# Optimization experiments

Measured on AMD Instinct MI355X. Metric: run time of the kernel, lower is better.

The kernel has to match this reference:

```python
import jax, jax.numpy as jnp
import numpy as np

B, H, E, V = 128, 1024, 1024, 40000
L, S, A = 256, 10, 10
L_S, L_A = 1.0, 1.0  # s_copy_lambda / a_copy_lambda
NEG = -1e24


def setup_inputs():
    key = jax.random.key(0)
    ks = jax.random.split(key, 32)
    n = lambda i, shape: jax.random.normal(ks[i], shape, dtype=jnp.float32)
    p = lambda i, shape: jax.random.normal(ks[i], shape, dtype=jnp.float32) * 0.02
    rnn_in = 3 * E + H  # embed + history ctx (H) + state ctx (E) + action ctx (E)
    return {
        "inp": n(0, (B, 1, E)),
        "hidden": n(1, (1, B, H)),
        "hs_vectors": n(2, (B, L, H)),
        "state_gumbel_prob": jax.random.uniform(ks[3], (B, S, V), dtype=jnp.float32),
        "state_gumbel_embed": n(4, (B, S, E)),
        "action_gumbel_prob": jax.random.uniform(ks[5], (B, A, V), dtype=jnp.float32),
        "action_gumbel_embed": n(6, (B, A, E)),
        "history_lens": jax.random.randint(ks[7], (B,), 1, L + 1),
        "history_word_indices": jax.random.randint(ks[8], (B, L), 0, V),
        # history word mlp-attention
        "Wq_hist": p(9, (H, H)), "bq_hist": jnp.zeros((H,), jnp.float32),
        "Wm_hist": p(10, (H, H)), "v_hist": p(11, (H,)),
        # init_s_attn / init_a_attn (query H, memory E)
        "Wq_s": p(12, (H, H)), "bq_s": jnp.zeros((H,), jnp.float32),
        "Wm_s": p(13, (E, H)), "v_s": p(14, (H,)),
        "Wq_a": p(15, (H, H)), "bq_a": jnp.zeros((H,), jnp.float32),
        "Wm_a": p(16, (E, H)), "v_a": p(17, (H,)),
        # sparse_copy_attn (memory E+1)
        "Wq_sc": p(18, (H, H)), "bq_sc": jnp.zeros((H,), jnp.float32),
        "Wm_sc": p(19, (E + 1, H)), "v_sc": p(20, (H,)),
        # GRU (torch layout: [3H, in], gate order r,z,n)
        "W_ih": p(21, (3 * H, rnn_in)), "W_hh": p(22, (3 * H, H)),
        "b_ih": jnp.zeros((3 * H,), jnp.float32), "b_hh": jnp.zeros((3 * H,), jnp.float32),
        # output projection
        "W_out": p(23, (H, V)), "b_out": jnp.zeros((V,), jnp.float32),
    }


def _mlp_scores(q, mem, Wq, bq, Wm, v):
    # q: [B,1,H], mem: [B,L,M] -> additive-attention logits [B,1,L]
    t = jnp.tanh((q @ Wq + bq) + (mem @ Wm))  # [B,L,H]
    return (t @ v)[:, None, :]


def reference(inp, hidden, hs_vectors, state_gumbel_prob, state_gumbel_embed,
              action_gumbel_prob, action_gumbel_embed, history_lens,
              history_word_indices, Wq_hist, bq_hist, Wm_hist, v_hist,
              Wq_s, bq_s, Wm_s, v_s, Wq_a, bq_a, Wm_a, v_a,
              Wq_sc, bq_sc, Wm_sc, v_sc, W_ih, W_hh, b_ih, b_hh, W_out, b_out):
    q0 = jnp.transpose(hidden, (1, 0, 2))  # [B,1,H]
    # --- history word attention (masked mlp attention) ---
    hist_scores = _mlp_scores(q0, hs_vectors, Wq_hist, bq_hist, Wm_hist, v_hist)
    valid = jnp.arange(L)[None, None, :] < history_lens[:, None, None]
    hist_scores = jnp.where(valid, hist_scores, NEG)
    c_his = jax.nn.softmax(hist_scores, axis=-1) @ hs_vectors  # [B,1,H]
    # --- init_consult over state / action gumbel embeddings ---
    sw = jax.nn.softmax(_mlp_scores(q0, state_gumbel_embed, Wq_s, bq_s, Wm_s, v_s), axis=-1)
    c_state = sw @ state_gumbel_embed  # [B,1,E]
    aw = jax.nn.softmax(_mlp_scores(q0, action_gumbel_embed, Wq_a, bq_a, Wm_a, v_a), axis=-1)
    c_action = aw @ action_gumbel_embed  # [B,1,E]
    x = jnp.concatenate([inp, c_his, c_state, c_action], axis=-1)[:, 0, :]  # [B,3E+H]
    # --- single-step GRU cell (torch semantics, gate order r,z,n) ---
    h0 = hidden[0]
    gi = x @ W_ih.T + b_ih
    gh = h0 @ W_hh.T + b_hh
    ir, iz, inn = jnp.split(gi, 3, axis=-1)
    hr, hz, hn = jnp.split(gh, 3, axis=-1)
    r = jax.nn.sigmoid(ir + hr)
    z = jax.nn.sigmoid(iz + hz)
    nact = jnp.tanh(inn + r * hn)
    h_new = (1.0 - z) * nact + z * h0  # [B,H]
    # --- vocab logits + copy logits, joint softmax ---
    gene_logits = h_new @ W_out + b_out  # [B,V]
    cq = h_new[:, None, :]
    hs_logits = jnp.einsum('bqh,blh->bql', cq, hs_vectors)[:, 0, :]  # dot attn, [B,L]
    s_tag = jnp.zeros((B, S, 1), jnp.float32)
    a_tag = jnp.ones((B, A, 1), jnp.float32)
    st_logits = _mlp_scores(cq, jnp.concatenate([state_gumbel_embed, s_tag], -1), Wq_sc, bq_sc, Wm_sc, v_sc)[:, 0, :]
    ac_logits = _mlp_scores(cq, jnp.concatenate([action_gumbel_embed, a_tag], -1), Wq_sc, bq_sc, Wm_sc, v_sc)[:, 0, :]
    all_logits = jnp.concatenate([gene_logits, hs_logits, st_logits, ac_logits], axis=-1)
    wp = jax.nn.softmax(all_logits, axis=-1)  # [B, V+L+S+A]
    gene_p = wp[:, :V]
    hs_w = wp[:, V:V + L]
    st_w = wp[:, V + L:V + L + S]
    ac_w = wp[:, V + L + S:]
    # --- copy-distribution mixing ---
    scp = jnp.einsum('bs,bsv->bv', st_w, state_gumbel_prob)
    acp = jnp.einsum('ba,bav->bv', ac_w, action_gumbel_prob)
    gene_p = gene_p + L_S * scp + L_A * acp
    copy_p = jnp.zeros((B, V), jnp.float32).at[jnp.arange(B)[:, None], history_word_indices].add(hs_w)
    out = jnp.log(gene_p + copy_p)[:, None, :]  # [B,1,V]
    return out, h_new[None]
```

## Files before the change

### kernel.cpp

```cpp
#include <hip/hip_runtime.h>
#include <stdint.h>

typedef __attribute__((ext_vector_type(4))) float f32x4;
typedef __attribute__((ext_vector_type(2))) unsigned int u32x2;
typedef __attribute__((ext_vector_type(4))) unsigned int u32x4;
typedef __attribute__((ext_vector_type(8))) short bf16x8;

#define BV (128*40000)

__device__ __forceinline__ unsigned rne_bf16(float f) {
    unsigned x = __float_as_uint(f);
    return ((x + 0x7FFFu + ((x >> 16) & 1u)) >> 16) & 0xFFFFu;
}
__device__ __forceinline__ unsigned pack2(float a, float b) {
    return rne_bf16(a) | (rne_bf16(b) << 16);
}
__device__ __forceinline__ float bf2f(unsigned u) {
    return __uint_as_float((u & 0xFFFFu) << 16);
}
__device__ __forceinline__ float sigm(float x) { return 1.0f / (1.0f + expf(-x)); }
__device__ __forceinline__ float ftanh(float x) {
    float e = __expf(2.0f * x);
    return 1.0f - 2.0f / (e + 1.0f);
}
// ... 7 lines not shown
struct BigArgs {
    const unsigned short *hs, *WmhT, *se, *ae, *WmsT, *WmaT, *WmscT;
    const float *qh_h, *bq_h, *v_h;
    const float *qh_s, *bq_s, *v_s;
    const float *qh_a, *bq_a, *v_a;
    float *hsc, *stsc, *acsc;
    unsigned short *mseh, *maeh;
};

__global__ __launch_bounds__(512, 1) void k_big(
    BigArgs a, int* __restrict__ ctr, const int* __restrict__ prefix,
    const int* __restrict__ ntp) {
    __shared__ unsigned short As[2][16384];
    __shared__ unsigned short Bs[2][16384];
    __shared__ int sTile;
    __shared__ int rows_tab[256];

    const int nTiles = ntp[0], Mp = ntp[1];
    const int t = threadIdx.x, lane = t & 63, wv = t >> 6;
    const int l16 = lane & 15, lq = lane >> 4;
    const int wm = wv >> 2, wn = wv & 3;
    const int srowL = t >> 3;
    const int gccA = ((t & 7) ^ (srowL & 7)) << 3;
    const int swz = l16 & 7;
    const int c0 = ((lq ^ swz) << 3);
    const int A0 = (wm << 13) + (l16 << 6);
    const int B0 = ((wn >> 1) << 13) + ((((wn & 1) << 6) + l16) << 6);

#define STQA(ktt, d, q) gload16(gAr[q] + (ktt) * 64, &As[d][((q) << 12) + (wv << 9)])
#define STQB(ktt, d, q) gload16(gB + ((size_t)(q) << 16) + (ktt) * 64, &Bs[d][((q) << 12) + (wv << 9)])

    for (;;) {
        __syncthreads();
        if (t == 0) sTile = atomicAdd(ctr, 1);
        __syncthreads();
        const int wg = sTile;
        if (wg >= nTiles) return;

        const unsigned short *Abase, *Bt;
        const float *rb = nullptr, *cb = nullptr, *vv = nullptr;
        float* out = nullptr;
        unsigned short* outh = nullptr;
        int m0, n0, vrows, cls;
        if (wg < 40) {
            cls = 0;
            int op = wg / 20, r = wg - op * 20;
            int mt = r >> 2, nt2 = r & 3;
            if (op == 0) { Abase = a.se; Bt = a.WmsT; rb = a.qh_s; cb = a.bq_s; vv = a.v_s; out = a.stsc; }
            else         { Abase = a.ae; Bt = a.WmaT; rb = a.qh_a; cb = a.bq_a; vv = a.v_a; out = a.acsc; }
            m0 = mt << 8; n0 = nt2 << 8; vrows = 256;
        } else if (wg < 80) {
            cls = 1;
            int r = wg - 40;
// ... 24 lines not shown
                        if (prefix[mid] <= g) lo = mid; else hi = mid;
                    }
                    rid = (lo << 8) + (g - prefix[lo]);
                } else {
                    rid = 0;
                }
            }
            rows_tab[t] = rid;
        }
        __syncthreads();

        const unsigned short* gAr[4];
#pragma unroll
        for (int q = 0; q < 4; ++q)
            gAr[q] = Abase + ((size_t)rows_tab[srowL + (q << 6)] << 10) + gccA;
        const unsigned short* gB = Bt + (size_t)(n0 + srowL) * 1024 + gccA;

        f32x4 acc[8][4];
#pragma unroll
        for (int i = 0; i < 8; ++i)
#pragma unroll
            for (int j = 0; j < 4; ++j) acc[i][j] = (f32x4){0.f, 0.f, 0.f, 0.f};

        STQA(0, 0, 0); STQA(0, 0, 2);
        STQB(0, 0, 0); STQB(0, 0, 1); STQB(0, 0, 2); STQB(0, 0, 3);
        STQA(0, 0, 1); STQA(0, 0, 3);
        __builtin_amdgcn_sched_barrier(0);
        asm volatile("s_waitcnt vmcnt(2)" ::: "memory");
        __builtin_amdgcn_s_barrier();
        __builtin_amdgcn_sched_barrier(0);

        for (int kt = 0; kt < 16; ++kt) {
            const int cur = kt & 1, dn = cur ^ 1, kn = kt + 1;
            const bool pre = kt < 15;
            const unsigned short* ab = As[cur];
            const unsigned short* bb = Bs[cur];
            bf16x8 bk0[4], bk1[4], af[4];
            if (pre) { STQA(kn, dn, 0); STQA(kn, dn, 2); }
#pragma unroll
            for (int nf = 0; nf < 4; ++nf) bk0[nf] = *(const bf16x8*)(bb + B0 + (nf << 10) + c0);
#pragma unroll
            for (int mf = 0; mf < 4; ++mf) af[mf] = *(const bf16x8*)(ab + A0 + (mf << 10) + c0);
            __builtin_amdgcn_s_setprio(1);
#pragma unroll
            for (int mf = 0; mf < 4; ++mf)
#pragma unroll
                for (int nf = 0; nf < 4; ++nf)
                    acc[mf][nf] = __builtin_amdgcn_mfma_f32_16x16x32_bf16(af[mf], bk0[nf], acc[mf][nf], 0, 0, 0);
            __builtin_amdgcn_s_setprio(0);
            if (pre) { STQB(kn, dn, 0); STQB(kn, dn, 1); }
#pragma unroll
            for (int nf = 0; nf < 4; ++nf) bk1[nf] = *(const bf16x8*)(bb + B0 + (nf << 10) + (c0 ^ 32));
#pragma unroll
            for (int mf = 0; mf < 4; ++mf) af[mf] = *(const bf16x8*)(ab + A0 + (mf << 10) + (c0 ^ 32));
            __builtin_amdgcn_s_setprio(1);
#pragma unroll
            for (int mf = 0; mf < 4; ++mf)
#pragma unroll
                for (int nf = 0; nf < 4; ++nf)
                    acc[mf][nf] = __builtin_amdgcn_mfma_f32_16x16x32_bf16(af[mf], bk1[nf], acc[mf][nf], 0, 0, 0);
            __builtin_amdgcn_s_setprio(0);
            if (pre) { STQB(kn, dn, 2); STQB(kn, dn, 3); }
            __builtin_amdgcn_sched_barrier(0);
            if (pre) asm volatile("s_waitcnt vmcnt(6)" ::: "memory");
            else     asm volatile("s_waitcnt vmcnt(0)" ::: "memory");
            __builtin_amdgcn_s_barrier();
            __builtin_amdgcn_sched_barrier(0);
#pragma unroll
            for (int mf = 0; mf < 4; ++mf) af[mf] = *(const bf16x8*)(ab + A0 + ((4 + mf) << 10) + c0);
            __builtin_amdgcn_s_setprio(1);
#pragma unroll
            for (int mf = 0; mf < 4; ++mf)
#pragma unroll
                for (int nf = 0; nf < 4; ++nf)
                    acc[4 + mf][nf] = __builtin_amdgcn_mfma_f32_16x16x32_bf16(af[mf], bk0[nf], acc[4 + mf][nf], 0, 0, 0);
            __builtin_amdgcn_s_setprio(0);
            if (pre) { STQA(kn, dn, 1); STQA(kn, dn, 3); }
#pragma unroll
            for (int mf = 0; mf < 4; ++mf) af[mf] = *(const bf16x8*)(ab + A0 + ((4 + mf) << 10) + (c0 ^ 32));
            __builtin_amdgcn_s_setprio(1);
#pragma unroll
            for (int mf = 0; mf < 4; ++mf)
#pragma unroll
                for (int nf = 0; nf < 4; ++nf)
                    acc[4 + mf][nf] = __builtin_amdgcn_mfma_f32_16x16x32_bf16(af[mf], bk1[nf], acc[4 + mf][nf], 0, 0, 0);
            __builtin_amdgcn_s_setprio(0);
            __builtin_amdgcn_sched_barrier(0);
            if (pre) asm volatile("s_waitcnt vmcnt(2)" ::: "memory");
            else     asm volatile("s_waitcnt vmcnt(0)" ::: "memory");
            __builtin_amdgcn_s_barrier();
            __builtin_amdgcn_sched_barrier(0);
        }

        if (cls == 1) {
            int gcs4[4];
#pragma unroll
            for (int nf = 0; nf < 4; ++nf) gcs4[nf] = n0 + (wn << 6) + (nf << 4) + l16;
#pragma unroll
            for (int mf = 0; mf < 8; ++mf) {
#pragma unroll
                for (int r = 0; r < 4; ++r) {
                    int grow = m0 + (wm << 7) + (mf << 4) + (lq << 2) + r;
#pragma unroll
                    for (int nf = 0; nf < 4; ++nf)
                        outh[(size_t)grow * 1024 + gcs4[nf]] = (unsigned short)rne_bf16(acc[mf][nf][r]);
                }
            }
        } else {
            float cbv[4], vvv[4];
            int gcs[4];
#pragma unroll
            for (int nf = 0; nf < 4; ++nf) {
                int gc = n0 + (wn << 6) + (nf << 4) + l16;
                gcs[nf] = gc; cbv[nf] = cb[gc]; vvv[nf] = vv[gc];
// ... 3 lines not shown
                int rloc = (wm << 7) + (mf << 4);
                if (rloc < vrows) {
#pragma unroll
                    for (int r = 0; r < 4; ++r) {
                        int lrow = rloc + (lq << 2) + r;
                        if (lrow >= vrows) continue;
                        int gr = m0 + lrow;
                        int bidx = (cls == 2) ? (rows_tab[lrow] >> 8) : (gr / 10);
                        const float* rbp = rb + ((size_t)bidx << 10);
                        float s = 0.f;
#pragma unroll
                        for (int nf = 0; nf < 4; ++nf) {
                            float x = acc[mf][nf][r] + rbp[gcs[nf]] + cbv[nf];
                            s += ftanh(x) * vvv[nf];
                        }
#pragma unroll
                        for (int m2 = 1; m2 < 16; m2 <<= 1) s += __shfl_xor(s, m2, 64);
                        if (l16 == 0) atomicAdd(&out[gr], s);
                    }
                }
            }
        }
    }
#undef STQA
#undef STQB
}

__device__ __forceinline__ void mgemm2(
    const unsigned short* __restrict__ A, const unsigned short* __restrict__ Bt,
    float* __restrict__ out,
    int m0, int n0, int kb, int ke, int ldk, int ldc)
{
    __shared__ unsigned short As[2][4096];
    __shared__ unsigned short Bs[2][4096];
    const int t = threadIdx.x, lane = t & 63, wv = t >> 6;
    const int l16 = lane & 15, lq = lane >> 4;
    const int wm = wv >> 1, wn = wv & 1;

    const int srow = lane >> 2, scol = (lane & 3) << 3;
    const unsigned short* gA0 = A + (size_t)(m0 + (wv << 4) + srow) * ldk + kb + scol;
    const unsigned short* gA1 = gA0 + (size_t)64 * ldk;
    const unsigned short* gB0 = Bt + (size_t)(n0 + (wv << 4) + srow) * ldk + kb + scol;
    const unsigned short* gB1 = gB0 + (size_t)64 * ldk;
    unsigned short* lA0 = &As[0][wv << 9];
    unsigned short* lA1 = &As[0][(wv + 4) << 9];
    unsigned short* lB0 = &Bs[0][wv << 9];
    unsigned short* lB1 = &Bs[0][(wv + 4) << 9];

// ... 23 lines not shown
#pragma unroll
        for (int i = 0; i < 4; ++i)
            bfv[i] = *(const bf16x8*)(bb + (((wn << 6) + (i << 4) + l16) << 5) + (lq << 3));
#pragma unroll
        for (int mf = 0; mf < 4; ++mf)
#pragma unroll
            for (int nf = 0; nf < 4; ++nf)
                acc[mf][nf] = __builtin_amdgcn_mfma_f32_16x16x32_bf16(af[mf], bfv[nf], acc[mf][nf], 0, 0, 0);
    }

#pragma unroll
    for (int mf = 0; mf < 4; ++mf) {
        int gr0 = m0 + (wm << 6) + (mf << 4) + (lq << 2);
#pragma unroll
        for (int nf = 0; nf < 4; ++nf) {
            int gc = n0 + (wn << 6) + (nf << 4) + l16;
#pragma unroll
            for (int r = 0; r < 4; ++r)
                atomicAdd(&out[(size_t)(gr0 + r) * ldc + gc], acc[mf][nf][r]);
        }
    }
}

__device__ __forceinline__ void gene_body(
    const unsigned short* __restrict__ hnb, const float* __restrict__ Wout,
    const float* __restrict__ b_out, float* __restrict__ out, int n0)
{
    __shared__ unsigned short As[2][4096];
    __shared__ unsigned short Bs[2][4096];
    const int t = threadIdx.x, lane = t & 63, wv = t >> 6;
    const int l16 = lane & 15, lq = lane >> 4;
    const int wm = wv >> 1, wn = wv & 1;

    const int srow = lane >> 2, scol = (lane & 3) << 3;
    const unsigned short* gA0 = hnb + (size_t)((wv << 4) + srow) * 1024 + scol;
    const unsigned short* gA1 = gA0 + (size_t)64 * 1024;
    unsigned short* lA0 = &As[0][wv << 9];
    unsigned short* lA1 = &As[0][(wv + 4) << 9];

    const int bn = t & 127, kh = t >> 7;
    const bool ok = (n0 + bn) < 40000;
    const float* gB = Wout + (size_t)(kh * 16) * 40000 + (n0 + bn);

    f32x4 acc[4][4];
#pragma unroll
    for (int i = 0; i < 4; ++i)
// ... 41 lines not shown
            int gc = n0 + (wn << 6) + (nf << 4) + l16;
            if (gc < 40000) {
                float bo = b_out[gc];
#pragma unroll
                for (int r = 0; r < 4; ++r)
                    out[(size_t)(gr0 + r) * 40000 + gc] = acc[mf][nf][r] + bo;
            }
        }
    }
}

__global__ __launch_bounds__(256) void k_qh4(
    const unsigned short* q0, const unsigned short* W0, const unsigned short* W1,
    const unsigned short* W2, float* o0, float* o1, float* o2) {
    const unsigned short* W = W0; float* o = o0;
    if (blockIdx.z == 1) { W = W1; o = o1; }
    if (blockIdx.z == 2) { W = W2; o = o2; }
    int kb = blockIdx.y << 8;
    mgemm2(q0, W, o, 0, blockIdx.x * 128, kb, kb + 256, 1024, 1024);
}

__global__ __launch_bounds__(256) void k_gigh2(
    const unsigned short* xb, const unsigned short* q0,
    const unsigned short* Wih, const unsigned short* Whh, float* gi, float* gh) {
    if (blockIdx.z == 0) {
        int kb = blockIdx.y << 9;
        mgemm2(xb, Wih, gi, 0, blockIdx.x * 128, kb, kb + 512, 4096, 3072);
    } else {
        if (blockIdx.y >= 2) return;
        int kb = blockIdx.y << 9;
        mgemm2(q0, Whh, gh, 0, blockIdx.x * 128, kb, kb + 512, 1024, 3072);
    }
}

__global__ __launch_bounds__(256) void k_geneR(
    const unsigned short* __restrict__ hnb, const float* __restrict__ Wout,
    const float* __restrict__ b_out, float* __restrict__ out,
    const float* __restrict__ sprob, const float* __restrict__ aprob,
    const float* __restrict__ wtil, float* __restrict__ R) {
    int id = blockIdx.x;
    if (id < 313) {
        gene_body(hnb, Wout, b_out, out, id << 7);
        return;
    }
    int rid = id - 313;
    int b = rid / 40, ch = rid - b * 40;
    int t = threadIdx.x;
    __shared__ float wsb[20];
    if (t < 20) wsb[t] = wtil[b * 20 + t];
    __syncthreads();
    if (t >= 250) return;
    int v4 = ch * 250 + t;
    size_t base = (size_t)b * 10000 + v4;
    f32x4 r = {0.f, 0.f, 0.f, 0.f};
#pragma unroll
    for (int s = 0; s < 10; ++s) {
        f32x4 pv = ((const f32x4*)sprob)[((size_t)b * 10 + s) * 10000 + v4];
        f32x4 av = ((const f32x4*)aprob)[((size_t)b * 10 + s) * 10000 + v4];
        float ws = wsb[s], wa = wsb[10 + s];
#pragma unroll
        for (int j = 0; j < 4; ++j) r[j] += ws * pv[j] + wa * av[j];
    }
    ((f32x4*)R)[base] = r;
}

struct PrepArgs {
    const float* cs[6]; unsigned short* cd[6]; int pre[7];
    const float* ts[8]; unsigned short* td[8];
    const int* lens; int* prefix; int* nt;
};
__global__ __launch_bounds__(256) void k_prep(PrepArgs a) {
    int bid = blockIdx.x, t = threadIdx.x;
    if (bid < 2048) {
        __shared__ float tile[64][65];
        int z = bid >> 8, rem = bid & 255, y = rem >> 4, x = rem & 15;
        const float* in = a.ts[z];
        unsigned short* ot = a.td[z];
        int k0 = y << 6, n0 = x << 6;
        int tr = t >> 6, tc = t & 63;
#pragma unroll
        for (int i = 0; i < 16; ++i) {
            int r = (i << 2) + tr;
            tile[r][tc] = in[(size_t)(k0 + r) * 1024 + n0 + tc];
        }
        __syncthreads();
#pragma unroll
        for (int i = 0; i < 16; ++i) {
            int r = (i << 2) + tr;
            ot[(size_t)(n0 + r) * 1024 + k0 + tc] = (unsigned short)rne_bf16(tile[tc][r]);
        }
    } else if (bid == 2048) {
        __shared__ int sc[128];
        if (t < 128) sc[t] = a.lens[t];
        __syncthreads();
        for (int off = 1; off < 128; off <<= 1) {
            int x = (t >= off && t < 128) ? sc[t - off] : 0;
            __syncthreads();
            if (t < 128) sc[t] += x;
            __syncthreads();
        }
        if (t == 0) a.prefix[0] = 0;
        if (t < 128) a.prefix[t + 1] = sc[t];
        if (t == 127) {
            int Mp = sc[127];
            a.nt[0] = 80 + (((Mp + 255) >> 8) << 2);
            a.nt[1] = Mp;
        }
    } else {
        int total = a.pre[6];
        for (int i = (bid - 2049) * 256 + t; i < total; i += 2048 * 256) {
            int seg = 0;
            while (i >= a.pre[seg + 1]) ++seg;
            int loc = i - a.pre[seg];
            const f32x4* s4 = (const f32x4*)a.cs[seg] + (size_t)loc * 2;
            f32x4 q0 = s4[0], q1 = s4[1];
            ((u32x4*)a.cd[seg])[loc] =
                (u32x4){pack2(q0[0],q0[1]), pack2(q0[2],q0[3]), pack2(q1[0],q1[1]), pack2(q1[2],q1[3])};
        }
    }
}

__device__ __forceinline__ void softmax10(const float* src, float* dst) {
    float m = src[0];
    for (int i = 1; i < 10; ++i) m = fmaxf(m, src[i]);
    float z = 0.f, e[10];
    for (int i = 0; i < 10; ++i) { e[i] = expf(src[i] - m); z += e[i]; }
    float iz = 1.0f / z;
    for (int i = 0; i < 10; ++i) dst[i] = e[i] * iz;
}

__global__ __launch_bounds__(256) void k_ctx(
    const float* __restrict__ scores, const int* __restrict__ lens,
// ... 36 lines not shown
        a2 += wl * bf2f(u[1]); a3 += wl * bf2f(u[1] >> 16);
    }
    *((u32x2*)(xb + (size_t)b * 4096 + 1024) + t) = (u32x2){pack2(a0, a1), pack2(a2, a3)};
    float cs0=0,cs1=0,cs2=0,cs3=0, ca0=0,ca1=0,ca2=0,ca3=0;
#pragma unroll
    for (int q = 0; q < 10; ++q) {
        u32x2 us = *((const u32x2*)(se + ((size_t)b * 10 + q) * 1024) + t);
        u32x2 ua = *((const u32x2*)(ae + ((size_t)b * 10 + q) * 1024) + t);
        float ws = sw[q], wa = aw[q];
        cs0 += ws * bf2f(us[0]); cs1 += ws * bf2f(us[0] >> 16);
        cs2 += ws * bf2f(us[1]); cs3 += ws * bf2f(us[1] >> 16);
        ca0 += wa * bf2f(ua[0]); ca1 += wa * bf2f(ua[0] >> 16);
        ca2 += wa * bf2f(ua[1]); ca3 += wa * bf2f(ua[1] >> 16);
    }
    *((u32x2*)(xb + (size_t)b * 4096 + 2048) + t) = (u32x2){pack2(cs0, cs1), pack2(cs2, cs3)};
    *((u32x2*)(xb + (size_t)b * 4096 + 3072) + t) = (u32x2){pack2(ca0, ca1), pack2(ca2, ca3)};
}

__global__ __launch_bounds__(1024) void k_gruhsl(
    const float* __restrict__ gi, const float* __restrict__ gh,
    const float* __restrict__ b_ih, const float* __restrict__ b_hh,
    const float* __restrict__ h0, float* __restrict__ hnew,
    unsigned short* __restrict__ hnb,
    const unsigned short* __restrict__ hs, float* __restrict__ hsl,
    const unsigned short* __restrict__ WqscT, float* __restrict__ qsc) {
    int b = blockIdx.x, y = blockIdx.y, j = threadIdx.x;
    size_t i = (size_t)b * 1024 + j;
    const float* gib = gi + (size_t)b * 3072;
    const float* ghb = gh + (size_t)b * 3072;
    float r = sigm(gib[j] + b_ih[j] + ghb[j] + b_hh[j]);
    float z = sigm(gib[1024 + j] + b_ih[1024 + j] + ghb[1024 + j] + b_hh[1024 + j]);
    float hn = ghb[2048 + j] + b_hh[2048 + j];
    float n = tanhf(gib[2048 + j] + b_ih[2048 + j] + r * hn);
    float h = (1.0f - z) * n + z * h0[i];
    if (y == 0) {
        hnew[i] = h;
        hnb[i] = (unsigned short)rne_bf16(h);
    }
    __shared__ float hsm[1024];
    hsm[j] = h;
    __syncthreads();
    {
        float acn = 0.f;
        const u32x4* wr = (const u32x4*)(WqscT + ((size_t)j << 10));
        int st = y << 6;
#pragma unroll 4
        for (int k8 = st; k8 < st + 64; ++k8) {
            u32x4 u = wr[k8];
            const float* hp = hsm + (k8 << 3);
            acn += hp[0]*bf2f(u[0]) + hp[1]*bf2f(u[0]>>16)
                 + hp[2]*bf2f(u[1]) + hp[3]*bf2f(u[1]>>16)
                 + hp[4]*bf2f(u[2]) + hp[5]*bf2f(u[2]>>16)
                 + hp[6]*bf2f(u[3]) + hp[7]*bf2f(u[3]>>16);
        }
        atomicAdd(&qsc[(size_t)b * 1024 + j], acn);
    }
    int wave = j >> 6, lane = j & 63;
    float hr[16];
#pragma unroll
    for (int k = 0; k < 16; ++k) hr[k] = hsm[lane * 16 + k];
    for (int l = (y << 7) + wave; l < (y << 7) + 128; l += 16) {
        const u32x4* row = (const u32x4*)(hs + ((size_t)b * 256 + l) * 1024);
        u32x4 u0 = row[lane * 2], u1 = row[lane * 2 + 1];
        float s = hr[0]*bf2f(u0[0]) + hr[1]*bf2f(u0[0]>>16) + hr[2]*bf2f(u0[1]) + hr[3]*bf2f(u0[1]>>16)
                + hr[4]*bf2f(u0[2]) + hr[5]*bf2f(u0[2]>>16) + hr[6]*bf2f(u0[3]) + hr[7]*bf2f(u0[3]>>16)
                + hr[8]*bf2f(u1[0]) + hr[9]*bf2f(u1[0]>>16) + hr[10]*bf2f(u1[1]) + hr[11]*bf2f(u1[1]>>16)
                + hr[12]*bf2f(u1[2]) + hr[13]*bf2f(u1[2]>>16) + hr[14]*bf2f(u1[3]) + hr[15]*bf2f(u1[3]>>16);
#pragma unroll
        for (int msk = 1; msk < 64; msk <<= 1) s += __shfl_xor(s, msk, 64);
        if (lane == 0) hsl[b * 256 + l] = s;
    }
}

__global__ __launch_bounds__(256) void k_stacep(
    const unsigned short* __restrict__ mseh, const unsigned short* __restrict__ maeh,
    const float* __restrict__ qsc, const float* __restrict__ bq_sc,
    const float* __restrict__ v_sc, const float* __restrict__ tagrow,
    float* __restrict__ stlg, float* __restrict__ aclg,
    float* __restrict__ mtil, float* __restrict__ wtil) {
    int b = blockIdx.x, t = threadIdx.x, w = t >> 6, lane = t & 63;
    __shared__ float res[20];
    const float* qb = qsc + (size_t)b * 1024;
    for (int r = w; r < 20; r += 4) {
        bool ac = r >= 10;
        int s = ac ? r - 10 : r;
        const unsigned short* mm = (ac ? maeh : mseh) + ((size_t)b * 10 + s) * 1024;
        float acc = 0.f;
#pragma unroll
        for (int j2 = 0; j2 < 16; ++j2) {
            int c = lane + (j2 << 6);
            float x = bf2f(mm[c]) + qb[c] + bq_sc[c];
            if (ac) x += tagrow[c];
            acc += ftanh(x) * v_sc[c];
        }
#pragma unroll
        for (int m2 = 1; m2 < 64; m2 <<= 1) acc += __shfl_xor(acc, m2, 64);
        if (lane == 0) res[r] = acc;
    }
    __syncthreads();
    if (t < 10) stlg[b * 10 + t] = res[t];
    if (t >= 64 && t < 74) aclg[b * 10 + (t - 64)] = res[10 + (t - 64)];
    if (t == 128) {
        float mt = res[0];
        for (int i2 = 1; i2 < 20; ++i2) mt = fmaxf(mt, res[i2]);
        mtil[b] = mt;
        for (int i2 = 0; i2 < 20; ++i2) wtil[b * 20 + i2] = expf(res[i2] - mt);
    }
}

__global__ __launch_bounds__(256) void k_smsc(
    const float* __restrict__ gene, const float* __restrict__ hsl,
    const float* __restrict__ stl, const float* __restrict__ acl,
    const int* __restrict__ hwi,
    float* __restrict__ mbuf, float* __restrict__ zbuf, float* __restrict__ copyp) {
    int b = blockIdx.x, t = threadIdx.x;
    __shared__ float red[256];
    const f32x4* g4 = (const f32x4*)(gene + (size_t)b * 40000);
    float mx = -3.0e38f;
    for (int i = t; i < 10000; i += 256) {
        f32x4 q = g4[i];
        mx = fmaxf(mx, fmaxf(fmaxf(q[0], q[1]), fmaxf(q[2], q[3])));
    }
    float hv = hsl[b * 256 + t];
    mx = fmaxf(mx, hv);
    if (t < 10) mx = fmaxf(mx, fmaxf(stl[b * 10 + t], acl[b * 10 + t]));
    red[t] = mx; __syncthreads();
    for (int s = 128; s > 0; s >>= 1) { if (t < s) red[t] = fmaxf(red[t], red[t + s]); __syncthreads(); }
    float m = red[0];
    __syncthreads();
    float sum = 0.f;
    for (int i = t; i < 10000; i += 256) {
        f32x4 q = g4[i];
        sum += expf(q[0]-m) + expf(q[1]-m) + expf(q[2]-m) + expf(q[3]-m);
    }
    sum += expf(hv - m);
    if (t < 10) sum += expf(stl[b * 10 + t] - m) + expf(acl[b * 10 + t] - m);
    red[t] = sum; __syncthreads();
    for (int s = 128; s > 0; s >>= 1) { if (t < s) red[t] += red[t + s]; __syncthreads(); }
    float Z = red[0];
    if (t == 0) { mbuf[b] = m; zbuf[b] = Z; }
    float wv = expf(hv - m) / Z;
    atomicAdd(copyp + (size_t)b * 40000 + hwi[b * 256 + t], wv);
}

__global__ __launch_bounds__(256) void k_final(
    float* __restrict__ gene_out, const float* __restrict__ copyp,
    const float* __restrict__ R, const float* __restrict__ mbuf,
    const float* __restrict__ zbuf, const float* __restrict__ mtil) {
    int b = blockIdx.y, t = threadIdx.x;
    int v4 = blockIdx.x * 256 + t;
    if (v4 < 10000) {
        float m = mbuf[b], iz = 1.0f / zbuf[b];
        float sb = expf(mtil[b] - m) * iz;
        size_t base = (size_t)b * 10000 + v4;
        f32x4 g = ((const f32x4*)gene_out)[base];
        f32x4 c = ((const f32x4*)copyp)[base];
        f32x4 rr = ((const f32x4*)R)[base];
        f32x4 r;
#pragma unroll
        for (int j = 0; j < 4; ++j)
            r[j] = logf(expf(g[j] - m) * iz + c[j] + rr[j] * sb);
        ((f32x4*)gene_out)[base] = r;
    }
}

#define OFF_QH_H  0
#define OFF_QH_S  131072
#define OFF_QH_A  262144
#define OFF_QSC   393216
#define OFF_GI    524288
#define OFF_GH    917504
#define OFF_HSC   1310720
#define OFF_STSC  1343488
#define OFF_ACSC  1344768
#define OFF_STLG  1346048
#define OFF_ACLG  1347328
#define OFF_CTR   1348608
#define OFF_PFX   1348736
#define OFF_NT    1348904
#define ZERO_FLOATS 1348936
#define OFF_HSL   1348992
#define OFF_M     1381760
#define OFF_Z     1381888
#define OFF_COPY  1382016
#define OFF_MTIL  6502016
#define OFF_WTIL  6502144
#define FLOAT_TOTAL 6504704
#define SO_HS     0
#define SO_SE     33554432
#define SO_AE     34865152
#define SO_Q0     36175872
#define SO_X      36306944
#define SO_HNB    36831232
#define SO_WQHT   36962304
#define SO_WQST   38010880
#define SO_WQAT   39059456
#define SO_WQSCT  40108032
#define SO_WMHT   41156608
#define SO_WMST   42205184
#define SO_WMAT   43253760
#define SO_WMSCT  44302336
#define SO_WIH    45350912
#define SO_WHH    57933824
#define SO_MSE    61079552
#define SO_MAE    62390272

extern "C" void kernel_launch(void* const* d_in, const int* in_sizes, int n_in,
                              void* d_out, int out_size, void* d_ws, size_t ws_size,
                              hipStream_t stream) {
    const float* inp     = (const float*)d_in[0];
    const float* hidden  = (const float*)d_in[1];
    const float* hs      = (const float*)d_in[2];
    const float* sprob   = (const float*)d_in[3];
    const float* se      = (const float*)d_in[4];
    const float* aprob   = (const float*)d_in[5];
    const float* ae      = (const float*)d_in[6];
    const int*   lens    = (const int*)d_in[7];
    const int*   hwi     = (const int*)d_in[8];
    const float* Wq_hist = (const float*)d_in[9];
    const float* bq_hist = (const float*)d_in[10];
    const float* Wm_hist = (const float*)d_in[11];
    const float* v_hist  = (const float*)d_in[12];
    const float* Wq_s    = (const float*)d_in[13];
    const float* bq_s    = (const float*)d_in[14];
    const float* Wm_s    = (const float*)d_in[15];
    const float* v_s     = (const float*)d_in[16];
    const float* Wq_a    = (const float*)d_in[17];
    const float* bq_a    = (const float*)d_in[18];
// ... 1 lines not shown
    const float* v_a     = (const float*)d_in[20];
    const float* Wq_sc   = (const float*)d_in[21];
    const float* bq_sc   = (const float*)d_in[22];
    const float* Wm_sc   = (const float*)d_in[23];
    const float* v_sc    = (const float*)d_in[24];
    const float* W_ih    = (const float*)d_in[25];
    const float* W_hh    = (const float*)d_in[26];
    const float* b_ih    = (const float*)d_in[27];
    const float* b_hh    = (const float*)d_in[28];
    const float* W_out   = (const float*)d_in[29];
    const float* b_out   = (const float*)d_in[30];

    float* out  = (float*)d_out;
    float* w    = (float*)d_ws;
    float* hnew = out + BV;
    unsigned short* sb = (unsigned short*)(w + FLOAT_TOTAL);

    float* qh_h = w + OFF_QH_H;  float* qh_s = w + OFF_QH_S;  float* qh_a = w + OFF_QH_A;
    float* qsc  = w + OFF_QSC;   float* gi   = w + OFF_GI;    float* gh   = w + OFF_GH;
    float* hsc  = w + OFF_HSC;   float* stsc = w + OFF_STSC;  float* acsc = w + OFF_ACSC;
    float* stlg = w + OFF_STLG;  float* aclg = w + OFF_ACLG;
    float* hsl  = w + OFF_HSL;   float* mbuf = w + OFF_M;     float* zbuf = w + OFF_Z;
    float* copyp = w + OFF_COPY;
    float* mtil = w + OFF_MTIL;  float* wtil = w + OFF_WTIL;
    int*   ctr  = (int*)(w + OFF_CTR);
    int*   pfx  = (int*)(w + OFF_PFX);
    int*   ntb  = (int*)(w + OFF_NT);

    unsigned short* hs_bf = sb + SO_HS;   unsigned short* se_bf = sb + SO_SE;
    unsigned short* ae_bf = sb + SO_AE;   unsigned short* q0_bf = sb + SO_Q0;
    unsigned short* x_bf  = sb + SO_X;    unsigned short* hnb   = sb + SO_HNB;
    unsigned short* WqhT  = sb + SO_WQHT; unsigned short* WqsT  = sb + SO_WQST;
    unsigned short* WqaT  = sb + SO_WQAT; unsigned short* WqscT = sb + SO_WQSCT;
    unsigned short* WmhT  = sb + SO_WMHT; unsigned short* WmsT  = sb + SO_WMST;
    unsigned short* WmaT  = sb + SO_WMAT; unsigned short* WmscT = sb + SO_WMSCT;
    unsigned short* WihB  = sb + SO_WIH;  unsigned short* WhhB  = sb + SO_WHH;
    unsigned short* mseh  = sb + SO_MSE;  unsigned short* maeh  = sb + SO_MAE;
    float* Rbuf = (float*)(sb + SO_WIH);

    dim3 blk(256);

    hipMemsetAsync(w, 0, (size_t)ZERO_FLOATS * 4, stream);
    hipMemsetAsync(copyp, 0, (size_t)BV * 4, stream);

    PrepArgs pa;
    pa.cs[0]=hs; pa.cs[1]=se; pa.cs[2]=ae; pa.cs[3]=hidden; pa.cs[4]=W_ih; pa.cs[5]=W_hh;
    pa.cd[0]=hs_bf; pa.cd[1]=se_bf; pa.cd[2]=ae_bf; pa.cd[3]=q0_bf; pa.cd[4]=WihB; pa.cd[5]=WhhB;
    pa.pre[0]=0; pa.pre[1]=4194304; pa.pre[2]=4358144; pa.pre[3]=4521984;
    pa.pre[4]=4538368; pa.pre[5]=6111232; pa.pre[6]=6504448;
    pa.ts[0]=Wq_hist; pa.ts[1]=Wq_s; pa.ts[2]=Wq_a; pa.ts[3]=Wq_sc;
    pa.ts[4]=Wm_hist; pa.ts[5]=Wm_s; pa.ts[6]=Wm_a; pa.ts[7]=Wm_sc;
    pa.td[0]=WqhT; pa.td[1]=WqsT; pa.td[2]=WqaT; pa.td[3]=WqscT;
    pa.td[4]=WmhT; pa.td[5]=WmsT; pa.td[6]=WmaT; pa.td[7]=WmscT;
    pa.lens = lens; pa.prefix = pfx; pa.nt = ntb;
    k_prep<<<dim3(4097), blk, 0, stream>>>(pa);

    k_qh4<<<dim3(8, 4, 3), blk, 0, stream>>>(q0_bf, WqhT, WqsT, WqaT, qh_h, qh_s, qh_a);

    BigArgs ba;
    ba.hs = hs_bf; ba.WmhT = WmhT; ba.se = se_bf; ba.ae = ae_bf;
    ba.WmsT = WmsT; ba.WmaT = WmaT; ba.WmscT = WmscT;
    ba.qh_h = qh_h; ba.bq_h = bq_hist; ba.v_h = v_hist;
    ba.qh_s = qh_s; ba.bq_s = bq_s; ba.v_s = v_s;
    ba.qh_a = qh_a; ba.bq_a = bq_a; ba.v_a = v_a;
    ba.hsc = hsc; ba.stsc = stsc; ba.acsc = acsc;
    ba.mseh = mseh; ba.maeh = maeh;
    k_big<<<dim3(256), dim3(512), 0, stream>>>(ba, ctr, pfx, ntb);

    k_ctx<<<dim3(128), blk, 0, stream>>>(hsc, lens, pfx, hs_bf, inp, stsc, acsc, se_bf, ae_bf, x_bf);
    k_gigh2<<<dim3(24, 8, 2), blk, 0, stream>>>(x_bf, q0_bf, WihB, WhhB, gi, gh);
    k_gruhsl<<<dim3(128, 2), dim3(1024), 0, stream>>>(gi, gh, b_ih, b_hh, hidden, hnew, hnb,
                                                      hs_bf, hsl, WqscT, qsc);
    k_stacep<<<dim3(128), blk, 0, stream>>>(mseh, maeh, qsc, bq_sc, v_sc,
                                            Wm_sc + (size_t)1024 * 1024, stlg, aclg, mtil, wtil);
    k_geneR<<<dim3(313 + 5120), blk, 0, stream>>>(hnb, W_out, b_out, out, sprob, aprob, wtil, Rbuf);
    k_smsc<<<dim3(128), blk, 0, stream>>>(out, hsl, stlg, aclg, hwi, mbuf, zbuf, copyp);
    k_final<<<dim3(40, 128), blk, 0, stream>>>(out, copyp, Rbuf, mbuf, zbuf, mtil);

    (void)in_sizes; (void)n_in; (void)out_size; (void)ws_size;
}
```

Measured before the change: 561.6 us.

## Restructure pipeline: simpler k_big loop, fp32 GRU weights, fused qsc+gene, fold copy mixing into final

```diff
diff --git a/kernel.cpp b/kernel.cpp
--- a/kernel.cpp
+++ b/kernel.cpp
@@ -53,13 +53,20 @@
     const int wm = wv >> 2, wn = wv & 3;
     const int srowL = t >> 3;
     const int gccA = ((t & 7) ^ (srowL & 7)) << 3;
-    const int swz = l16 & 7;
-    const int c0 = ((lq ^ swz) << 3);
+    const int sw = l16 & 7;
+    const int c0 = ((lq ^ sw) << 3);
     const int A0 = (wm << 13) + (l16 << 6);
     const int B0 = ((wn >> 1) << 13) + ((((wn & 1) << 6) + l16) << 6);
 
-#define STQA(ktt, d, q) gload16(gAr[q] + (ktt) * 64, &As[d][((q) << 12) + (wv << 9)])
-#define STQB(ktt, d, q) gload16(gB + ((size_t)(q) << 16) + (ktt) * 64, &Bs[d][((q) << 12) + (wv << 9)])
+#define STAGE(kt, d)                                                          \
+    {                                                                         \
+        _Pragma("unroll")                                                     \
+        for (int q_ = 0; q_ < 4; ++q_) {                                      \
+            int lo_ = (q_ << 12) + (wv << 9);                                 \
+            gload16(gAr[q_] + (kt) * 64, &As[d][lo_]);                        \
+            gload16(gB + (size_t)(q_ << 16) + (kt) * 64, &Bs[d][lo_]);        \
+        }                                                                     \
+    }
 
     for (;;) {
         __syncthreads();
@@ -130,74 +137,43 @@
 #pragma unroll
             for (int j = 0; j < 4; ++j) acc[i][j] = (f32x4){0.f, 0.f, 0.f, 0.f};
 
-        STQA(0, 0, 0); STQA(0, 0, 2);
-        STQB(0, 0, 0); STQB(0, 0, 1); STQB(0, 0, 2); STQB(0, 0, 3);
-        STQA(0, 0, 1); STQA(0, 0, 3);
-        __builtin_amdgcn_sched_barrier(0);
-        asm volatile("s_waitcnt vmcnt(2)" ::: "memory");
-        __builtin_amdgcn_s_barrier();
-        __builtin_amdgcn_sched_barrier(0);
-
+        STAGE(0, 0);
         for (int kt = 0; kt < 16; ++kt) {
-            const int cur = kt & 1, dn = cur ^ 1, kn = kt + 1;
-            const bool pre = kt < 15;
+            int cur = kt & 1;
+            if (kt < 15) {
+                STAGE(kt + 1, cur ^ 1);
+                asm volatile("s_waitcnt vmcnt(8)" ::: "memory");
+            } else {
+                asm volatile("s_waitcnt vmcnt(0)" ::: "memory");
+            }
+            __builtin_amdgcn_s_barrier();
+            __builtin_amdgcn_sched_barrier(0);
+
             const unsigned short* ab = As[cur];
             const unsigned short* bb = Bs[cur];
-            bf16x8 bk0[4], bk1[4], af[4];
-            if (pre) { STQA(kn, dn, 0); STQA(kn, dn, 2); }
-#pragma unroll
-            for (int nf = 0; nf < 4; ++nf) bk0[nf] = *(const bf16x8*)(bb + B0 + (nf << 10) + c0);
-#pragma unroll
-            for (int mf = 0; mf < 4; ++mf) af[mf] = *(const bf16x8*)(ab + A0 + (mf << 10) + c0);
-            __builtin_amdgcn_s_setprio(1);
-#pragma unroll
-            for (int mf = 0; mf < 4; ++mf)
-#pragma unroll
-                for (int nf = 0; nf < 4; ++nf)
-                    acc[mf][nf] = __builtin_amdgcn_mfma_f32_16x16x32_bf16(af[mf], bk0[nf], acc[mf][nf], 0, 0, 0);
-            __builtin_amdgcn_s_setprio(0);
-            if (pre) { STQB(kn, dn, 0); STQB(kn, dn, 1); }
-#pragma unroll
-            for (int nf = 0; nf < 4; ++nf) bk1[nf] = *(const bf16x8*)(bb + B0 + (nf << 10) + (c0 ^ 32));
-#pragma unroll
-            for (int mf = 0; mf < 4; ++mf) af[mf] = *(const bf16x8*)(ab + A0 + (mf << 10) + (c0 ^ 32));
-            __builtin_amdgcn_s_setprio(1);
-#pragma unroll
-            for (int mf = 0; mf < 4; ++mf)
-#pragma unroll
-                for (int nf = 0; nf < 4; ++nf)
-                    acc[mf][nf] = __builtin_amdgcn_mfma_f32_16x16x32_bf16(af[mf], bk1[nf], acc[mf][nf], 0, 0, 0);
-            __builtin_amdgcn_s_setprio(0);
-            if (pre) { STQB(kn, dn, 2); STQB(kn, dn, 3); }
+            if (vrows > (wm << 7)) {
+                bf16x8 bf0[4], bf1[4];
+#pragma unroll
+                for (int nf = 0; nf < 4; ++nf) {
+                    bf0[nf] = *(const bf16x8*)(bb + B0 + (nf << 10) + c0);
+                    bf1[nf] = *(const bf16x8*)(bb + B0 + (nf << 10) + (c0 ^ 32));
+                }
+#pragma unroll
+                for (int mf = 0; mf < 8; ++mf) {
+                    if ((wm << 7) + (mf << 4) < vrows) {
+                        bf16x8 a0 = *(const bf16x8*)(ab + A0 + (mf << 10) + c0);
+                        bf16x8 a1 = *(const bf16x8*)(ab + A0 + (mf << 10) + (c0 ^ 32));
+#pragma unroll
+                        for (int nf = 0; nf < 4; ++nf)
+                            acc[mf][nf] = __builtin_amdgcn_mfma_f32_16x16x32_bf16(a0, bf0[nf], acc[mf][nf], 0, 0, 0);
+#pragma unroll
+                        for (int nf = 0; nf < 4; ++nf)
+                            acc[mf][nf] = __builtin_amdgcn_mfma_f32_16x16x32_bf16(a1, bf1[nf], acc[mf][nf], 0, 0, 0);
+                    }
+                }
+            }
             __builtin_amdgcn_sched_barrier(0);
-            if (pre) asm volatile("s_waitcnt vmcnt(6)" ::: "memory");
-            else     asm volatile("s_waitcnt vmcnt(0)" ::: "memory");
             __builtin_amdgcn_s_barrier();
-            __builtin_amdgcn_sched_barrier(0);
-#pragma unroll
-            for (int mf = 0; mf < 4; ++mf) af[mf] = *(const bf16x8*)(ab + A0 + ((4 + mf) << 10) + c0);
-            __builtin_amdgcn_s_setprio(1);
-#pragma unroll
-            for (int mf = 0; mf < 4; ++mf)
-#pragma unroll
-                for (int nf = 0; nf < 4; ++nf)
-                    acc[4 + mf][nf] = __builtin_amdgcn_mfma_f32_16x16x32_bf16(af[mf], bk0[nf], acc[4 + mf][nf], 0, 0, 0);
-            __builtin_amdgcn_s_setprio(0);
-            if (pre) { STQA(kn, dn, 1); STQA(kn, dn, 3); }
-#pragma unroll
-            for (int mf = 0; mf < 4; ++mf) af[mf] = *(const bf16x8*)(ab + A0 + ((4 + mf) << 10) + (c0 ^ 32));
-            __builtin_amdgcn_s_setprio(1);
-#pragma unroll
-            for (int mf = 0; mf < 4; ++mf)
-#pragma unroll
-                for (int nf = 0; nf < 4; ++nf)
-                    acc[4 + mf][nf] = __builtin_amdgcn_mfma_f32_16x16x32_bf16(af[mf], bk1[nf], acc[4 + mf][nf], 0, 0, 0);
-            __builtin_amdgcn_s_setprio(0);
-            __builtin_amdgcn_sched_barrier(0);
-            if (pre) asm volatile("s_waitcnt vmcnt(2)" ::: "memory");
-            else     asm volatile("s_waitcnt vmcnt(0)" ::: "memory");
-            __builtin_amdgcn_s_barrier();
-            __builtin_amdgcn_sched_barrier(0);
         }
 
         if (cls == 1) {
@@ -247,8 +223,7 @@
             }
         }
     }
-#undef STQA
-#undef STQB
+#undef STAGE
 }
 
 __device__ __forceinline__ void mgemm2(
@@ -318,6 +293,81 @@
     }
 }
 
+__device__ __forceinline__ void mgemm2f(
+    const unsigned short* __restrict__ A, const float* __restrict__ Bf,
+    float* __restrict__ out,
+    int m0, int n0, int kb, int ke, int ldkA, int ldkB, int ldc)
+{
+    __shared__ unsigned short As[2][4096];
+    __shared__ unsigned short Bs[2][4096];
+    const int t = threadIdx.x, lane = t & 63, wv = t >> 6;
+    const int l16 = lane & 15, lq = lane >> 4;
+    const int wm = wv >> 1, wn = wv & 1;
+
+    const int srow = lane >> 2, scol = (lane & 3) << 3;
+    const unsigned short* gA0 = A + (size_t)(m0 + (wv << 4) + srow) * ldkA + kb + scol;
+    const unsigned short* gA1 = gA0 + (size_t)64 * ldkA;
+    unsigned short* lA0 = &As[0][wv << 9];
+    unsigned short* lA1 = &As[0][(wv + 4) << 9];
+
+    const int bn = t >> 1, kh = (t & 1) << 4;
+    const float* gB = Bf + (size_t)(n0 + bn) * ldkB + kb + kh;
+
+    f32x4 acc[4][4];
+#pragma unroll
+    for (int i = 0; i < 4; ++i)
+#pragma unroll
+        for (int j = 0; j < 4; ++j) acc[i][j] = (f32x4){0.f, 0.f, 0.f, 0.f};
+
+    auto stageB = [&](int buf, int ko) {
+        const float* s = gB + ko;
+        f32x4 f0 = *(const f32x4*)(s);
+        f32x4 f1 = *(const f32x4*)(s + 4);
+        f32x4 f2 = *(const f32x4*)(s + 8);
+        f32x4 f3 = *(const f32x4*)(s + 12);
+        u32x4* d = (u32x4*)&Bs[buf][bn * 32 + kh];
+        d[0] = (u32x4){pack2(f0[0],f0[1]), pack2(f0[2],f0[3]), pack2(f1[0],f1[1]), pack2(f1[2],f1[3])};
+        d[1] = (u32x4){pack2(f2[0],f2[1]), pack2(f2[2],f2[3]), pack2(f3[0],f3[1]), pack2(f3[2],f3[3])};
+    };
+
+    const int NS = (ke - kb) >> 5;
+    gload16(gA0, lA0); gload16(gA1, lA1); stageB(0, 0);
+    for (int s = 0; s < NS; ++s) {
+        __syncthreads();
+        if (s + 1 < NS) {
+            const int nb = (s + 1) & 1, ko = (s + 1) << 5;
+            gload16(gA0 + ko, lA0 + (nb << 12)); gload16(gA1 + ko, lA1 + (nb << 12));
+            stageB(nb, ko);
+        }
+        const unsigned short* ab = As[s & 1];
+        const unsigned short* bb = Bs[s & 1];
+        bf16x8 af[4], bfv[4];
+#pragma unroll
+        for (int i = 0; i < 4; ++i)
+            af[i] = *(const bf16x8*)(ab + (((wm << 6) + (i << 4) + l16) << 5) + (lq << 3));
+#pragma unroll
+        for (int i = 0; i < 4; ++i)
+            bfv[i] = *(const bf16x8*)(bb + (((wn << 6) + (i << 4) + l16) << 5) + (lq << 3));
+#pragma unroll
+        for (int mf = 0; mf < 4; ++mf)
+#pragma unroll
+            for (int nf = 0; nf < 4; ++nf)
+                acc[mf][nf] = __builtin_amdgcn_mfma_f32_16x16x32_bf16(af[mf], bfv[nf], acc[mf][nf], 0, 0, 0);
+    }
+
+#pragma unroll
+    for (int mf = 0; mf < 4; ++mf) {
+        int gr0 = m0 + (wm << 6) + (mf << 4) + (lq << 2);
+#pragma unroll
+        for (int nf = 0; nf < 4; ++nf) {
+            int gc = n0 + (wn << 6) + (nf << 4) + l16;
+#pragma unroll
+            for (int r = 0; r < 4; ++r)
+                atomicAdd(&out[(size_t)(gr0 + r) * ldc + gc], acc[mf][nf][r]);
+        }
+    }
+}
+
 __device__ __forceinline__ void gene_body(
     const unsigned short* __restrict__ hnb, const float* __restrict__ Wout,
     const float* __restrict__ b_out, float* __restrict__ out, int n0)
@@ -405,50 +455,31 @@
 
 __global__ __launch_bounds__(256) void k_gigh2(
     const unsigned short* xb, const unsigned short* q0,
-    const unsigned short* Wih, const unsigned short* Whh, float* gi, float* gh) {
+    const float* Wih, const float* Whh, float* gi, float* gh) {
     if (blockIdx.z == 0) {
         int kb = blockIdx.y << 9;
-        mgemm2(xb, Wih, gi, 0, blockIdx.x * 128, kb, kb + 512, 4096, 3072);
+        mgemm2f(xb, Wih, gi, 0, blockIdx.x * 128, kb, kb + 512, 4096, 4096, 3072);
     } else {
         if (blockIdx.y >= 2) return;
         int kb = blockIdx.y << 9;
-        mgemm2(q0, Whh, gh, 0, blockIdx.x * 128, kb, kb + 512, 1024, 3072);
-    }
-}
-
-__global__ __launch_bounds__(256) void k_geneR(
-    const unsigned short* __restrict__ hnb, const float* __restrict__ Wout,
-    const float* __restrict__ b_out, float* __restrict__ out,
-    const float* __restrict__ sprob, const float* __restrict__ aprob,
-    const float* __restrict__ wtil, float* __restrict__ R) {
+        mgemm2f(q0, Whh, gh, 0, blockIdx.x * 128, kb, kb + 512, 1024, 1024, 3072);
+    }
+}
+
+__global__ __launch_bounds__(256) void k_qsc_gene(
+    const unsigned short* hnb, const unsigned short* WqscT, float* qsc,
+    const float* Wout, const float* b_out, float* out) {
     int id = blockIdx.x;
-    if (id < 313) {
-        gene_body(hnb, Wout, b_out, out, id << 7);
-        return;
-    }
-    int rid = id - 313;
-    int b = rid / 40, ch = rid - b * 40;
-    int t = threadIdx.x;
-    __shared__ float wsb[20];
-    if (t < 20) wsb[t] = wtil[b * 20 + t];
-    __syncthreads();
-    if (t >= 250) return;
-    int v4 = ch * 250 + t;
-    size_t base = (size_t)b * 10000 + v4;
-    f32x4 r = {0.f, 0.f, 0.f, 0.f};
-#pragma unroll
-    for (int s = 0; s < 10; ++s) {
-        f32x4 pv = ((const f32x4*)sprob)[((size_t)b * 10 + s) * 10000 + v4];
-        f32x4 av = ((const f32x4*)aprob)[((size_t)b * 10 + s) * 10000 + v4];
-        float ws = wsb[s], wa = wsb[10 + s];
-#pragma unroll
-        for (int j = 0; j < 4; ++j) r[j] += ws * pv[j] + wa * av[j];
-    }
-    ((f32x4*)R)[base] = r;
+    if (id < 16) {
+        int x = id & 7, kb = (id >> 3) << 9;
+        mgemm2(hnb, WqscT, qsc, 0, x * 128, kb, kb + 512, 1024, 1024);
+    } else {
+        gene_body(hnb, Wout, b_out, out, (id - 16) << 7);
+    }
 }
 
 struct PrepArgs {
-    const float* cs[6]; unsigned short* cd[6]; int pre[7];
+    const float* cs[4]; unsigned short* cd[4]; int pre[5];
     const float* ts[8]; unsigned short* td[8];
     const int* lens; int* prefix; int* nt;
 };
@@ -490,7 +521,7 @@
             a.nt[1] = Mp;
         }
     } else {
-        int total = a.pre[6];
+        int total = a.pre[4];
         for (int i = (bid - 2049) * 256 + t; i < total; i += 2048 * 256) {
             int seg = 0;
             while (i >= a.pre[seg + 1]) ++seg;
@@ -573,8 +604,7 @@
     const float* __restrict__ b_ih, const float* __restrict__ b_hh,
     const float* __restrict__ h0, float* __restrict__ hnew,
     unsigned short* __restrict__ hnb,
-    const unsigned short* __restrict__ hs, float* __restrict__ hsl,
-    const unsigned short* __restrict__ WqscT, float* __restrict__ qsc) {
+    const unsigned short* __restrict__ hs, float* __restrict__ hsl) {
     int b = blockIdx.x, y = blockIdx.y, j = threadIdx.x;
     size_t i = (size_t)b * 1024 + j;
     const float* gib = gi + (size_t)b * 3072;
@@ -591,21 +621,6 @@
     __shared__ float hsm[1024];
     hsm[j] = h;
     __syncthreads();
-    {
-        float acn = 0.f;
-        const u32x4* wr = (const u32x4*)(WqscT + ((size_t)j << 10));
-        int st = y << 6;
-#pragma unroll 4
-        for (int k8 = st; k8 < st + 64; ++k8) {
-            u32x4 u = wr[k8];
-            const float* hp = hsm + (k8 << 3);
-            acn += hp[0]*bf2f(u[0]) + hp[1]*bf2f(u[0]>>16)
-                 + hp[2]*bf2f(u[1]) + hp[3]*bf2f(u[1]>>16)
-                 + hp[4]*bf2f(u[2]) + hp[5]*bf2f(u[2]>>16)
-                 + hp[6]*bf2f(u[3]) + hp[7]*bf2f(u[3]>>16);
-        }
-        atomicAdd(&qsc[(size_t)b * 1024 + j], acn);
-    }
     int wave = j >> 6, lane = j & 63;
     float hr[16];
 #pragma unroll
@@ -627,8 +642,7 @@
     const unsigned short* __restrict__ mseh, const unsigned short* __restrict__ maeh,
     const float* __restrict__ qsc, const float* __restrict__ bq_sc,
     const float* __restrict__ v_sc, const float* __restrict__ tagrow,
-    float* __restrict__ stlg, float* __restrict__ aclg,
-    float* __restrict__ mtil, float* __restrict__ wtil) {
+    float* __restrict__ stlg, float* __restrict__ aclg) {
     int b = blockIdx.x, t = threadIdx.x, w = t >> 6, lane = t & 63;
     __shared__ float res[20];
     const float* qb = qsc + (size_t)b * 1024;
@@ -651,12 +665,6 @@
     __syncthreads();
     if (t < 10) stlg[b * 10 + t] = res[t];
     if (t >= 64 && t < 74) aclg[b * 10 + (t - 64)] = res[10 + (t - 64)];
-    if (t == 128) {
-        float mt = res[0];
-        for (int i2 = 1; i2 < 20; ++i2) mt = fmaxf(mt, res[i2]);
-        mtil[b] = mt;
-        for (int i2 = 0; i2 < 20; ++i2) wtil[b * 20 + i2] = expf(res[i2] - mt);
-    }
 }
 
 __global__ __launch_bounds__(256) void k_smsc(
@@ -696,21 +704,34 @@
 
 __global__ __launch_bounds__(256) void k_final(
     float* __restrict__ gene_out, const float* __restrict__ copyp,
-    const float* __restrict__ R, const float* __restrict__ mbuf,
-    const float* __restrict__ zbuf, const float* __restrict__ mtil) {
+    const float* __restrict__ sprob, const float* __restrict__ aprob,
+    const float* __restrict__ stl, const float* __restrict__ acl,
+    const float* __restrict__ mbuf, const float* __restrict__ zbuf) {
     int b = blockIdx.y, t = threadIdx.x;
+    __shared__ float sw[10], aw[10];
+    float m = mbuf[b], iz = 1.0f / zbuf[b];
+    if (t < 10) sw[t] = expf(stl[b * 10 + t] - m) * iz;
+    if (t >= 64 && t < 74) aw[t - 64] = expf(acl[b * 10 + (t - 64)] - m) * iz;
+    __syncthreads();
     int v4 = blockIdx.x * 256 + t;
     if (v4 < 10000) {
-        float m = mbuf[b], iz = 1.0f / zbuf[b];
-        float sb = expf(mtil[b] - m) * iz;
         size_t base = (size_t)b * 10000 + v4;
         f32x4 g = ((const f32x4*)gene_out)[base];
         f32x4 c = ((const f32x4*)copyp)[base];
-        f32x4 rr = ((const f32x4*)R)[base];
+        f32x4 acc;
+#pragma unroll
+        for (int j = 0; j < 4; ++j) acc[j] = expf(g[j] - m) * iz + c[j];
+#pragma unroll
+        for (int s = 0; s < 10; ++s) {
+            f32x4 pv = ((const f32x4*)sprob)[((size_t)b * 10 + s) * 10000 + v4];
+            f32x4 av = ((const f32x4*)aprob)[((size_t)b * 10 + s) * 10000 + v4];
+            float ws = sw[s], wa = aw[s];
+#pragma unroll
+            for (int j = 0; j < 4; ++j) acc[j] += ws * pv[j] + wa * av[j];
+        }
         f32x4 r;
 #pragma unroll
-        for (int j = 0; j < 4; ++j)
-            r[j] = logf(expf(g[j] - m) * iz + c[j] + rr[j] * sb);
+        for (int j = 0; j < 4; ++j) r[j] = logf(acc[j]);
         ((f32x4*)gene_out)[base] = r;
     }
 }
@@ -734,9 +755,7 @@
 #define OFF_M     1381760
 #define OFF_Z     1381888
 #define OFF_COPY  1382016
-#define OFF_MTIL  6502016
-#define OFF_WTIL  6502144
-#define FLOAT_TOTAL 6504704
+#define FLOAT_TOTAL 6502016
 #define SO_HS     0
 #define SO_SE     33554432
 #define SO_AE     34865152
@@ -751,10 +770,8 @@
 #define SO_WMST   42205184
 #define SO_WMAT   43253760
 #define SO_WMSCT  44302336
-#define SO_WIH    45350912
-#define SO_WHH    57933824
-#define SO_MSE    61079552
-#define SO_MAE    62390272
+#define SO_MSE    45350912
+#define SO_MAE    46661632
 
 extern "C" void kernel_launch(void* const* d_in, const int* in_sizes, int n_in,
                               void* d_out, int out_size, void* d_ws, size_t ws_size,
@@ -802,7 +819,6 @@
     float* stlg = w + OFF_STLG;  float* aclg = w + OFF_ACLG;
     float* hsl  = w + OFF_HSL;   float* mbuf = w + OFF_M;     float* zbuf = w + OFF_Z;
     float* copyp = w + OFF_COPY;
-    float* mtil = w + OFF_MTIL;  float* wtil = w + OFF_WTIL;
     int*   ctr  = (int*)(w + OFF_CTR);
     int*   pfx  = (int*)(w + OFF_PFX);
     int*   ntb  = (int*)(w + OFF_NT);
@@ -814,9 +830,7 @@
     unsigned short* WqaT  = sb + SO_WQAT; unsigned short* WqscT = sb + SO_WQSCT;
     unsigned short* WmhT  = sb + SO_WMHT; unsigned short* WmsT  = sb + SO_WMST;
     unsigned short* WmaT  = sb + SO_WMAT; unsigned short* WmscT = sb + SO_WMSCT;
-    unsigned short* WihB  = sb + SO_WIH;  unsigned short* WhhB  = sb + SO_WHH;
     unsigned short* mseh  = sb + SO_MSE;  unsigned short* maeh  = sb + SO_MAE;
-    float* Rbuf = (float*)(sb + SO_WIH);
 
     dim3 blk(256);
 
@@ -824,10 +838,9 @@
     hipMemsetAsync(copyp, 0, (size_t)BV * 4, stream);
 
     PrepArgs pa;
-    pa.cs[0]=hs; pa.cs[1]=se; pa.cs[2]=ae; pa.cs[3]=hidden; pa.cs[4]=W_ih; pa.cs[5]=W_hh;
-    pa.cd[0]=hs_bf; pa.cd[1]=se_bf; pa.cd[2]=ae_bf; pa.cd[3]=q0_bf; pa.cd[4]=WihB; pa.cd[5]=WhhB;
-    pa.pre[0]=0; pa.pre[1]=4194304; pa.pre[2]=4358144; pa.pre[3]=4521984;
-    pa.pre[4]=4538368; pa.pre[5]=6111232; pa.pre[6]=6504448;
+    pa.cs[0]=hs; pa.cs[1]=se; pa.cs[2]=ae; pa.cs[3]=hidden;
+    pa.cd[0]=hs_bf; pa.cd[1]=se_bf; pa.cd[2]=ae_bf; pa.cd[3]=q0_bf;
+    pa.pre[0]=0; pa.pre[1]=4194304; pa.pre[2]=4358144; pa.pre[3]=4521984; pa.pre[4]=4538368;
     pa.ts[0]=Wq_hist; pa.ts[1]=Wq_s; pa.ts[2]=Wq_a; pa.ts[3]=Wq_sc;
     pa.ts[4]=Wm_hist; pa.ts[5]=Wm_s; pa.ts[6]=Wm_a; pa.ts[7]=Wm_sc;
     pa.td[0]=WqhT; pa.td[1]=WqsT; pa.td[2]=WqaT; pa.td[3]=WqscT;
@@ -848,14 +861,13 @@
     k_big<<<dim3(256), dim3(512), 0, stream>>>(ba, ctr, pfx, ntb);
 
     k_ctx<<<dim3(128), blk, 0, stream>>>(hsc, lens, pfx, hs_bf, inp, stsc, acsc, se_bf, ae_bf, x_bf);
-    k_gigh2<<<dim3(24, 8, 2), blk, 0, stream>>>(x_bf, q0_bf, WihB, WhhB, gi, gh);
-    k_gruhsl<<<dim3(128, 2), dim3(1024), 0, stream>>>(gi, gh, b_ih, b_hh, hidden, hnew, hnb,
-                                                      hs_bf, hsl, WqscT, qsc);
+    k_gigh2<<<dim3(24, 8, 2), blk, 0, stream>>>(x_bf, q0_bf, W_ih, W_hh, gi, gh);
+    k_gruhsl<<<dim3(128, 2), dim3(1024), 0, stream>>>(gi, gh, b_ih, b_hh, hidden, hnew, hnb, hs_bf, hsl);
+    k_qsc_gene<<<dim3(329), blk, 0, stream>>>(hnb, WqscT, qsc, W_out, b_out, out);
     k_stacep<<<dim3(128), blk, 0, stream>>>(mseh, maeh, qsc, bq_sc, v_sc,
-                                            Wm_sc + (size_t)1024 * 1024, stlg, aclg, mtil, wtil);
-    k_geneR<<<dim3(313 + 5120), blk, 0, stream>>>(hnb, W_out, b_out, out, sprob, aprob, wtil, Rbuf);
+                                            Wm_sc + (size_t)1024 * 1024, stlg, aclg);
     k_smsc<<<dim3(128), blk, 0, stream>>>(out, hsl, stlg, aclg, hwi, mbuf, zbuf, copyp);
-    k_final<<<dim3(40, 128), blk, 0, stream>>>(out, copyp, Rbuf, mbuf, zbuf, mtil);
+    k_final<<<dim3(40, 128), blk, 0, stream>>>(out, copyp, sprob, aprob, stlg, aclg, mbuf, zbuf);
 
     (void)in_sizes; (void)n_in; (void)out_size; (void)ws_size;
 }
```

Result: faster. 549.0 us (-2.2%).
